# Optimization experiments

Measured on AMD Instinct MI355X. Metric: run time of the kernel, lower is better.

Reference implementation:

```python
import jax, jax.numpy as jnp
import numpy as np

ADAPTER_RATIO = 0.2


def setup_inputs() -> dict:
    key = jax.random.key(0)
    k1, k2, k3, k4, k5 = jax.random.split(key, 5)
    B, D, R, N_DOM, N_TXT = 16384, 1024, 256, 3, 1380
    image_features = jax.random.normal(k1, (B, D), dtype=jnp.float32)
    domain_labels = jax.random.randint(k2, (B,), 0, N_DOM, dtype=jnp.int64)
    W1 = jax.random.normal(k3, (N_DOM, D, R), dtype=jnp.float32) * 0.02
    W2 = jax.random.normal(k4, (N_DOM, R, D), dtype=jnp.float32) * 0.02
    txt = jax.random.normal(k5, (N_TXT, D), dtype=jnp.float32)
    # text features are L2-normalized at module init (encode_text then norm)
    text_features = txt / jnp.linalg.norm(txt, axis=-1, keepdims=True)
    logit_scale = jnp.asarray(np.log(1.0 / 0.07), dtype=jnp.float32)  # CLIP init
    return {
        "image_features": image_features,
        "domain_labels": domain_labels,
        "W1": W1,
        "W2": W2,
        "text_features": text_features,
        "logit_scale": logit_scale,
    }


def reference(image_features, domain_labels, W1, W2, text_features, logit_scale):
    # Domain-routed adapter MLP: run all n_domains experts (n is tiny), then
    # select the routed output per sample (equivalent to the per-sample loop).
    h = jax.nn.relu(jnp.einsum("bd,ndr->bnr", image_features, W1))  # [B,n,R]
    a = jax.nn.relu(jnp.einsum("bnr,nrd->bnd", h, W2))              # [B,n,D]
    idx = domain_labels[:, None, None]                                # [B,1,1]
    adapter_features = jnp.take_along_axis(a, idx, axis=1)[:, 0, :]   # [B,D]
    fused = ADAPTER_RATIO * adapter_features + (1.0 - ADAPTER_RATIO) * image_features
    fused = fused / jnp.linalg.norm(fused, axis=-1, keepdims=True)
    # text_features already normalized; concat over domains done upstream: [N_TXT, D]
    logits = jnp.exp(logit_scale) * (fused @ text_features.T)         # [B, N_TXT]
    return logits
```

## Files before the change

### kernel.cpp

```cpp
#include <hip/hip_runtime.h>
#include <hip/hip_bf16.h>
#include <math.h>

using bf16 = __hip_bfloat16;
typedef __attribute__((ext_vector_type(8))) short bf16x8;
typedef __attribute__((ext_vector_type(4))) float f32x4;
typedef __attribute__((ext_vector_type(4))) unsigned short us4;

#define GAS __attribute__((address_space(1)))
#define LAS __attribute__((address_space(3)))

__device__ __forceinline__ void gload_lds16(const bf16* g, bf16* lds) {
  __builtin_amdgcn_global_load_lds((const GAS void*)g, (LAS void*)lds, 16, 0, 0);
}
__device__ __forceinline__ float b2f(unsigned short u) {
  union { unsigned short s; bf16 b; } x; x.s = u; return __bfloat162float(x.b);
}

__global__ __launch_bounds__(256) void hist_k(const int* __restrict__ lab,
                                              int* __restrict__ blockHist) {
  const int blk = blockIdx.x, t = threadIdx.x;
  const int lane = t & 63, w = t >> 6;
  const int d = lab[blk * 256 + t];
  __shared__ int wc[4][3];
#pragma unroll
  for (int dd = 0; dd < 3; ++dd) {
    unsigned long long m = __ballot(d == dd);
    if (lane == 0) wc[w][dd] = __popcll(m);
  }
  __syncthreads();
  if (t < 3) blockHist[blk * 3 + t] = wc[0][t] + wc[1][t] + wc[2][t] + wc[3][t];
}

__global__ __launch_bounds__(256) void scan_k(const int* __restrict__ blockHist,
                                              int* __restrict__ blockOff,
                                              int* __restrict__ meta) {
  __shared__ int h[64][3];
  __shared__ int tot[3];
  const int t = threadIdx.x;
  if (t < 192) h[t / 3][t % 3] = blockHist[t];
  __syncthreads();
  if (t < 3) {
    int s = 0;
    for (int b = 0; b < 64; ++b) { int v = h[b][t]; h[b][t] = s; s += v; }
    tot[t] = s;
    meta[t] = s;
  }
  __syncthreads();
  if (t == 0) { meta[4] = 0; meta[5] = tot[0]; meta[6] = tot[0] + tot[1]; }
  if (t < 192) {
    int b = t / 3, d = t % 3;
    int base = (d == 0) ? 0 : (d == 1 ? tot[0] : tot[0] + tot[1]);
    blockOff[t] = base + h[b][d];
  }
}

__global__ __launch_bounds__(256) void scatter2_k(const int* __restrict__ lab,
                                                  const int* __restrict__ blockOff,
                                                  int* __restrict__ perm) {
  const int blk = blockIdx.x, t = threadIdx.x;
  const int lane = t & 63, w = t >> 6;
  const int i = blk * 256 + t;
  const int d = lab[i];
  __shared__ int wc[4][3];
  unsigned long long mymask = 0;
#pragma unroll
  for (int dd = 0; dd < 3; ++dd) {
    unsigned long long m = __ballot(d == dd);
    if (lane == 0) wc[w][dd] = __popcll(m);
    if (dd == d) mymask = m;
  }
  __syncthreads();
  int woff = 0;
  for (int ww = 0; ww < w; ++ww) woff += wc[ww][d];
  const unsigned long long lt = ((unsigned long long)1 << lane) - 1;
  const int rank = blockOff[blk * 3 + d] + woff + __popcll(mymask & lt);
  perm[rank] = i;
}

__global__ __launch_bounds__(256) void cvt_all_k(const float* __restrict__ x,
                                                 const float* __restrict__ W1,
                                                 const float* __restrict__ W2,
                                                 const float* __restrict__ txt,
                                                 bf16* __restrict__ Xb,
                                                 bf16* __restrict__ W1T,
                                                 bf16* __restrict__ W2T,
                                                 bf16* __restrict__ Tb) {
  const int nx = 16384 * 1024 / 4;
  const int n1 = 3 * 256 * 1024;
  const int n2 = n1 + 3 * 1024 * 256;
  const int n3 = n2 + 1536 * 1024;
  const int total = nx + n3;
  for (int i = blockIdx.x * 256 + threadIdx.x; i < total; i += 4096 * 256) {
    if (i < nx) {
      float4 v = ((const float4*)x)[i];
      bf16 t[4] = {__float2bfloat16(v.x), __float2bfloat16(v.y),
                   __float2bfloat16(v.z), __float2bfloat16(v.w)};
      ((us4*)Xb)[i] = *(const us4*)t;
      continue;
    }
    int j = i - nx;
    if (j < n1) {
      int d = j >> 18, rem = j & 262143;
      int r = rem >> 10, k = rem & 1023;
      W1T[j] = __float2bfloat16(W1[(size_t)d * 262144 + (size_t)k * 256 + r]);
    } else if (j < n2) {
      int jj = j - n1;
      int d = jj >> 18, rem = jj & 262143;
      int n = rem >> 8, k = rem & 255;
      W2T[jj] = __float2bfloat16(W2[(size_t)d * 262144 + (size_t)k * 1024 + n]);
    } else {
      int jj = j - n2;
      Tb[jj] = (jj < 1380 * 1024) ? __float2bfloat16(txt[jj]) : __float2bfloat16(0.f);
    }
  }
}

template <bool GATHER_A, int EPI, int NBLK>
__global__ __launch_bounds__(256) void gemm_bt(
    const bf16* __restrict__ A, const bf16* __restrict__ BT, bf16* __restrict__ Cv,
    const int* __restrict__ perm, const int* __restrict__ meta, int N,
    int K, int ldc, int Nvalid,
    const bf16* __restrict__ xb, float* __restrict__ ssp) {
  const int bid = blockIdx.x;
  const int xcd = bid & 7;
  const int seq = bid >> 3;
  const int nblkidx = seq % NBLK;
  const int dm = xcd + 8 * (seq / NBLK);
  const int dom = dm >> 7;
  const int mblk = dm & 127;

  const int cnt = meta[dom];
  const int base = meta[4 + dom];
  BT += (size_t)dom * N * K;

  const int m0 = mblk * 128;
  if (m0 >= cnt) return;
  const int n0 = nblkidx * 128;

  __shared__ bf16 sA[2][128][32];
  __shared__ bf16 sB[2][128][32];

  const int tid = threadIdx.x;
  const int wid = tid >> 6;
  const int lane = tid & 63;

  const int srow = (wid << 4) + (lane >> 2);
  const int skoff = (((lane & 3) ^ ((lane >> 2) & 3)) << 3);

  int p0 = m0 + srow;       if (p0 > cnt - 1) p0 = cnt - 1;
  int p1 = m0 + srow + 64;  if (p1 > cnt - 1) p1 = cnt - 1;
  long ar0, ar1;
  if (GATHER_A) { ar0 = perm[base + p0]; ar1 = perm[base + p1]; }
  else          { ar0 = base + p0;       ar1 = base + p1; }
  const bf16* a0 = A + (size_t)ar0 * K + skoff;
  const bf16* a1 = A + (size_t)ar1 * K + skoff;
  const bf16* b0 = BT + (size_t)(n0 + srow) * K + skoff;
  const bf16* b1 = BT + (size_t)(n0 + srow + 64) * K + skoff;

  const int fr = lane & 15;
  const int fq = lane >> 4;
  const int rchunk = (fq ^ (fr & 3)) << 3;

  f32x4 acc[4][4];
#pragma unroll
  for (int m = 0; m < 4; ++m)
#pragma unroll
    for (int n = 0; n < 4; ++n) acc[m][n] = (f32x4){0.f, 0.f, 0.f, 0.f};

  const int nk = K >> 5;
  auto stage = [&](int buf, int kt) {
    gload_lds16(a0 + kt * 32, &sA[buf][wid * 16][0]);
    gload_lds16(a1 + kt * 32, &sA[buf][wid * 16 + 64][0]);
    gload_lds16(b0 + kt * 32, &sB[buf][wid * 16][0]);
    gload_lds16(b1 + kt * 32, &sB[buf][wid * 16 + 64][0]);
  };

  stage(0, 0);
  __syncthreads();
  const int wr = wid >> 1, wc = wid & 1;
  for (int kt = 0; kt < nk; ++kt) {
    const int cur = kt & 1;
    if (kt + 1 < nk) stage(cur ^ 1, kt + 1);
    bf16x8 af[4], bfr[4];
#pragma unroll
    for (int m = 0; m < 4; ++m)
      af[m] = *(const bf16x8*)&sA[cur][wr * 64 + m * 16 + fr][rchunk];
#pragma unroll
    for (int n = 0; n < 4; ++n)
      bfr[n] = *(const bf16x8*)&sB[cur][wc * 64 + n * 16 + fr][rchunk];
#pragma unroll
    for (int m = 0; m < 4; ++m)
#pragma unroll
      for (int n = 0; n < 4; ++n)
        acc[m][n] = __builtin_amdgcn_mfma_f32_16x16x32_bf16(af[m], bfr[n], acc[m][n], 0, 0, 0);
    __syncthreads();
  }

  if (EPI == 0) {
#pragma unroll
    for (int m = 0; m < 4; ++m) {
#pragma unroll
      for (int r = 0; r < 4; ++r) {
        const int p = m0 + wr * 64 + m * 16 + fq * 4 + r;
        if (p < cnt) {
          const size_t crow = (size_t)(base + p);
#pragma unroll
          for (int n = 0; n < 4; ++n) {
            const int col = n0 + wc * 64 + n * 16 + fr;
            if (col < Nvalid)
              Cv[crow * (size_t)ldc + col] = __float2bfloat16(fmaxf(acc[m][n][r], 0.f));
          }
        }
      }
    }
  } else {
    __shared__ float ssred[128][2];
#pragma unroll
    for (int m = 0; m < 4; ++m) {
#pragma unroll
      for (int r = 0; r < 4; ++r) {
        const int lr = wr * 64 + m * 16 + fq * 4 + r;
        const int p = m0 + lr;
        float rowss = 0.f;
        if (p < cnt) {
          const size_t crow = (size_t)perm[base + p];
#pragma unroll
          for (int n = 0; n < 4; ++n) {
            const int col = n0 + wc * 64 + n * 16 + fr;
            const float g = 0.2f * fmaxf(acc[m][n][r], 0.f) +
                            0.8f * b2f(*(const unsigned short*)&xb[crow * 1024 + col]);
            Cv[crow * (size_t)ldc + col] = __float2bfloat16(g);
            rowss += g * g;
          }
        }
        rowss += __shfl_xor(rowss, 1, 16);
        rowss += __shfl_xor(rowss, 2, 16);
        rowss += __shfl_xor(rowss, 4, 16);
        rowss += __shfl_xor(rowss, 8, 16);
        if (fr == 0) ssred[lr][wc] = rowss;
      }
    }
    __syncthreads();
    if (tid < 128) {
      const int p = m0 + tid;
      if (p < cnt) {
        const int crow = perm[base + p];
        ssp[(size_t)nblkidx * 16384 + crow] = ssred[tid][0] + ssred[tid][1];
      }
    }
  }
}

__global__ __launch_bounds__(256, 2) void gemm3_occ(
    const bf16* __restrict__ A, const bf16* __restrict__ BT,
    float* __restrict__ C, const float* __restrict__ scale_ptr,
    const float* __restrict__ ssp) {
  extern __shared__ bf16 smem[];
  bf16* sA0 = smem;
  bf16* sB0 = smem + 16384;

  const int tid = threadIdx.x;
  const int lane = tid & 63, wid = tid >> 6;
  const int wr = wid >> 1, wc = wid & 1;
  const int fr = lane & 15, fq = lane >> 4;

  const int bid = blockIdx.x;
  const int x = bid & 7, seq = bid >> 3;
  const int mb = x * 16 + (seq >> 3), nb = seq & 7;
  const int m0 = mb << 7, n0 = nb * 192;

  auto STAGE = [&](int t) {
    const int s = t & 1, koff = t << 6;
    bf16* da = sA0 + (s << 13);
#pragma unroll
    for (int L = 0; L < 4; ++L) {
      const int idx = (L << 8) + tid;
      const int r = idx >> 3, c = idx & 7;
      gload_lds16(A + (size_t)(m0 + r) * 1024 + koff + ((c ^ (r & 7)) << 3),
                  da + ((idx & ~63) << 3));
    }
    bf16* db = sB0 + s * 12288;
#pragma unroll
    for (int L = 0; L < 6; ++L) {
      const int idx = (L << 8) + tid;
      const int r = idx >> 3, c = idx & 7;
      gload_lds16(BT + (size_t)(n0 + r) * 1024 + koff + ((c ^ (r & 7)) << 3),
                  db + ((idx & ~63) << 3));
    }
  };
  auto LDA = [&](int s, int kk, bf16x8* dst) {
    const bf16* base = sA0 + (s << 13);
#pragma unroll
    for (int m = 0; m < 4; ++m) {
      const int row = (wr << 6) + (m << 4) + fr;
      dst[m] = *(const bf16x8*)(base + (row << 6) + ((((kk << 2) + fq) ^ (fr & 7)) << 3));
    }
  };
  auto LDB = [&](int s, int kk, bf16x8* dst) {
    const bf16* base = sB0 + s * 12288;
#pragma unroll
    for (int n = 0; n < 6; ++n) {
      const int row = wc * 96 + (n << 4) + fr;
      dst[n] = *(const bf16x8*)(base + (row << 6) + ((((kk << 2) + fq) ^ (fr & 7)) << 3));
    }
  };

  f32x4 acc[4][6];
#pragma unroll
  for (int m = 0; m < 4; ++m)
#pragma unroll
    for (int n = 0; n < 6; ++n) acc[m][n] = (f32x4){0.f, 0.f, 0.f, 0.f};

  STAGE(0);
  __syncthreads();
  const int nt = 16;
  for (int t = 0; t < nt; ++t) {
    const int s = t & 1;
    if (t + 1 < nt) STAGE(t + 1);
    bf16x8 a0[4], a1[4], b0[6], b1[6];
    LDA(s, 0, a0); LDB(s, 0, b0);
    LDA(s, 1, a1); LDB(s, 1, b1);
#pragma unroll
    for (int m = 0; m < 4; ++m)
#pragma unroll
      for (int n = 0; n < 6; ++n)
        acc[m][n] = __builtin_amdgcn_mfma_f32_16x16x32_bf16(a0[m], b0[n], acc[m][n], 0, 0, 0);
#pragma unroll
    for (int m = 0; m < 4; ++m)
#pragma unroll
      for (int n = 0; n < 6; ++n)
        acc[m][n] = __builtin_amdgcn_mfma_f32_16x16x32_bf16(a1[m], b1[n], acc[m][n], 0, 0, 0);
    __syncthreads();
  }

  float* rlds = (float*)smem;
  if (tid < 128) {
    float s = 0.f;
#pragma unroll
    for (int b = 0; b < 8; ++b) s += ssp[b * 16384 + m0 + tid];
    rlds[tid] = rsqrtf(s);
  }
  __syncthreads();

  const float sc = expf(*scale_ptr);
#pragma unroll
  for (int m = 0; m < 4; ++m) {
    const int lrow = (wr << 6) + (m << 4) + (fq << 2);
    const int grow = m0 + lrow;
#pragma unroll
    for (int r = 0; r < 4; ++r) {
      const float rv = sc * rlds[lrow + r];
#pragma unroll
      for (int n = 0; n < 6; ++n) {
        const int gcol = n0 + wc * 96 + (n << 4) + fr;
        if (gcol < 1380) C[(size_t)(grow + r) * 1380 + gcol] = acc[m][n][r] * rv;
      }
    }
  }
}

extern "C" void kernel_launch(void* const* d_in, const int* in_sizes, int n_in,
                              void* d_out, int out_size, void* d_ws, size_t ws_size,
                              hipStream_t stream) {
  (void)in_sizes; (void)n_in; (void)out_size; (void)ws_size;
  const float* x    = (const float*)d_in[0];
  const int*   lab  = (const int*)d_in[1];
  const float* W1   = (const float*)d_in[2];
  const float* W2   = (const float*)d_in[3];
  const float* text = (const float*)d_in[4];
  const float* lsc  = (const float*)d_in[5];
  float* out = (float*)d_out;

  const int B = 16384, D = 1024, R = 256, NTP = 1536;

  char* p = (char*)d_ws;
  auto carve = [&](size_t bytes) {
    char* r = p;
    p += (bytes + 255) & ~(size_t)255;
    return r;
  };
  int*   meta  = (int*)carve(64);
  int*   bhist = (int*)carve(64 * 3 * 4);
  int*   boff  = (int*)carve(64 * 3 * 4);
  int*   perm  = (int*)carve((size_t)B * 4);
  float* ssp   = (float*)carve((size_t)8 * B * 4);
  bf16*  Xb    = (bf16*)carve((size_t)B * D * 2);
  bf16*  W1T   = (bf16*)carve((size_t)3 * R * D * 2);
  bf16*  W2T   = (bf16*)carve((size_t)3 * D * R * 2);
  bf16*  Tb    = (bf16*)carve((size_t)NTP * D * 2);
  bf16*  H     = (bf16*)carve((size_t)B * R * 2);
  bf16*  Fb    = (bf16*)carve((size_t)B * D * 2);

  hist_k<<<B / 256, 256, 0, stream>>>(lab, bhist);
  scan_k<<<1, 256, 0, stream>>>(bhist, boff, meta);
  scatter2_k<<<B / 256, 256, 0, stream>>>(lab, boff, perm);

  cvt_all_k<<<4096, 256, 0, stream>>>(x, W1, W2, text, Xb, W1T, W2T, Tb);

  gemm_bt<true, 0, 2><<<768, 256, 0, stream>>>(
      Xb, W1T, H, perm, meta, R, D, R, R, nullptr, nullptr);
  gemm_bt<false, 1, 8><<<3072, 256, 0, stream>>>(
      H, W2T, Fb, perm, meta, D, R, D, D, Xb, ssp);
  gemm3_occ<<<1024, 256, 81920, stream>>>(Fb, Tb, out, lsc, ssp);
}
```

Before: 162.4 us.

## Store image features in domain-sorted order and scatter only final logits

```diff
diff --git a/kernel.cpp b/kernel.cpp
--- a/kernel.cpp
+++ b/kernel.cpp
@@ -57,7 +57,8 @@
 
 __global__ __launch_bounds__(256) void scatter2_k(const int* __restrict__ lab,
                                                   const int* __restrict__ blockOff,
-                                                  int* __restrict__ perm) {
+                                                  int* __restrict__ perm,
+                                                  int* __restrict__ iperm) {
   const int blk = blockIdx.x, t = threadIdx.x;
   const int lane = t & 63, w = t >> 6;
   const int i = blk * 256 + t;
@@ -76,13 +77,15 @@
   const unsigned long long lt = ((unsigned long long)1 << lane) - 1;
   const int rank = blockOff[blk * 3 + d] + woff + __popcll(mymask & lt);
   perm[rank] = i;
+  iperm[i] = rank;
 }
 
 __global__ __launch_bounds__(256) void cvt_all_k(const float* __restrict__ x,
                                                  const float* __restrict__ W1,
                                                  const float* __restrict__ W2,
                                                  const float* __restrict__ txt,
-                                                 bf16* __restrict__ Xb,
+                                                 const int* __restrict__ iperm,
+                                                 bf16* __restrict__ Xbc,
                                                  bf16* __restrict__ W1T,
                                                  bf16* __restrict__ W2T,
                                                  bf16* __restrict__ Tb) {
@@ -93,10 +96,11 @@
   const int total = nx + n3;
   for (int i = blockIdx.x * 256 + threadIdx.x; i < total; i += 4096 * 256) {
     if (i < nx) {
+      const int row = i >> 8, c4 = i & 255;
       float4 v = ((const float4*)x)[i];
       bf16 t[4] = {__float2bfloat16(v.x), __float2bfloat16(v.y),
                    __float2bfloat16(v.z), __float2bfloat16(v.w)};
-      ((us4*)Xb)[i] = *(const us4*)t;
+      ((us4*)Xbc)[(size_t)iperm[row] * 256 + c4] = *(const us4*)t;
       continue;
     }
     int j = i - nx;
@@ -116,11 +120,10 @@
   }
 }
 
-template <bool GATHER_A, int EPI, int NBLK>
+template <int EPI, int NBLK>
 __global__ __launch_bounds__(256) void gemm_bt(
     const bf16* __restrict__ A, const bf16* __restrict__ BT, bf16* __restrict__ Cv,
-    const int* __restrict__ perm, const int* __restrict__ meta, int N,
-    int K, int ldc, int Nvalid,
+    const int* __restrict__ meta, int N, int K, int ldc, int Nvalid,
     const bf16* __restrict__ xb, float* __restrict__ ssp) {
   const int bid = blockIdx.x;
   const int xcd = bid & 7;
@@ -150,11 +153,8 @@
 
   int p0 = m0 + srow;       if (p0 > cnt - 1) p0 = cnt - 1;
   int p1 = m0 + srow + 64;  if (p1 > cnt - 1) p1 = cnt - 1;
-  long ar0, ar1;
-  if (GATHER_A) { ar0 = perm[base + p0]; ar1 = perm[base + p1]; }
-  else          { ar0 = base + p0;       ar1 = base + p1; }
-  const bf16* a0 = A + (size_t)ar0 * K + skoff;
-  const bf16* a1 = A + (size_t)ar1 * K + skoff;
+  const bf16* a0 = A + (size_t)(base + p0) * K + skoff;
+  const bf16* a1 = A + (size_t)(base + p1) * K + skoff;
   const bf16* b0 = BT + (size_t)(n0 + srow) * K + skoff;
   const bf16* b1 = BT + (size_t)(n0 + srow + 64) * K + skoff;
 
@@ -224,7 +224,7 @@
         const int p = m0 + lr;
         float rowss = 0.f;
         if (p < cnt) {
-          const size_t crow = (size_t)perm[base + p];
+          const size_t crow = (size_t)(base + p);
 #pragma unroll
           for (int n = 0; n < 4; ++n) {
             const int col = n0 + wc * 64 + n * 16 + fr;
@@ -244,10 +244,8 @@
     __syncthreads();
     if (tid < 128) {
       const int p = m0 + tid;
-      if (p < cnt) {
-        const int crow = perm[base + p];
-        ssp[(size_t)nblkidx * 16384 + crow] = ssred[tid][0] + ssred[tid][1];
-      }
+      if (p < cnt)
+        ssp[(size_t)nblkidx * 16384 + base + p] = ssred[tid][0] + ssred[tid][1];
     }
   }
 }
@@ -255,7 +253,7 @@
 __global__ __launch_bounds__(256, 2) void gemm3_occ(
     const bf16* __restrict__ A, const bf16* __restrict__ BT,
     float* __restrict__ C, const float* __restrict__ scale_ptr,
-    const float* __restrict__ ssp) {
+    const float* __restrict__ ssp, const int* __restrict__ perm) {
   extern __shared__ bf16 smem[];
   bf16* sA0 = smem;
   bf16* sB0 = smem + 16384;
@@ -335,11 +333,13 @@
   }
 
   float* rlds = (float*)smem;
+  int*   plds = (int*)((char*)smem + 512);
   if (tid < 128) {
     float s = 0.f;
 #pragma unroll
     for (int b = 0; b < 8; ++b) s += ssp[b * 16384 + m0 + tid];
     rlds[tid] = rsqrtf(s);
+    plds[tid] = perm[m0 + tid];
   }
   __syncthreads();
 
@@ -347,14 +347,14 @@
 #pragma unroll
   for (int m = 0; m < 4; ++m) {
     const int lrow = (wr << 6) + (m << 4) + (fq << 2);
-    const int grow = m0 + lrow;
 #pragma unroll
     for (int r = 0; r < 4; ++r) {
       const float rv = sc * rlds[lrow + r];
+      const size_t orow = (size_t)plds[lrow + r];
 #pragma unroll
       for (int n = 0; n < 6; ++n) {
         const int gcol = n0 + wc * 96 + (n << 4) + fr;
-        if (gcol < 1380) C[(size_t)(grow + r) * 1380 + gcol] = acc[m][n][r] * rv;
+        if (gcol < 1380) C[orow * 1380 + gcol] = acc[m][n][r] * rv;
       }
     }
   }
@@ -384,23 +384,24 @@
   int*   bhist = (int*)carve(64 * 3 * 4);
   int*   boff  = (int*)carve(64 * 3 * 4);
   int*   perm  = (int*)carve((size_t)B * 4);
+  int*   iperm = (int*)carve((size_t)B * 4);
   float* ssp   = (float*)carve((size_t)8 * B * 4);
-  bf16*  Xb    = (bf16*)carve((size_t)B * D * 2);
+  bf16*  Xbc   = (bf16*)carve((size_t)B * D * 2);
   bf16*  W1T   = (bf16*)carve((size_t)3 * R * D * 2);
   bf16*  W2T   = (bf16*)carve((size_t)3 * D * R * 2);
   bf16*  Tb    = (bf16*)carve((size_t)NTP * D * 2);
   bf16*  H     = (bf16*)carve((size_t)B * R * 2);
-  bf16*  Fb    = (bf16*)carve((size_t)B * D * 2);
+  bf16*  Fbc   = (bf16*)carve((size_t)B * D * 2);
 
   hist_k<<<B / 256, 256, 0, stream>>>(lab, bhist);
   scan_k<<<1, 256, 0, stream>>>(bhist, boff, meta);
-  scatter2_k<<<B / 256, 256, 0, stream>>>(lab, boff, perm);
-
-  cvt_all_k<<<4096, 256, 0, stream>>>(x, W1, W2, text, Xb, W1T, W2T, Tb);
-
-  gemm_bt<true, 0, 2><<<768, 256, 0, stream>>>(
-      Xb, W1T, H, perm, meta, R, D, R, R, nullptr, nullptr);
-  gemm_bt<false, 1, 8><<<3072, 256, 0, stream>>>(
-      H, W2T, Fb, perm, meta, D, R, D, D, Xb, ssp);
-  gemm3_occ<<<1024, 256, 81920, stream>>>(Fb, Tb, out, lsc, ssp);
-}
+  scatter2_k<<<B / 256, 256, 0, stream>>>(lab, boff, perm, iperm);
+
+  cvt_all_k<<<4096, 256, 0, stream>>>(x, W1, W2, text, iperm, Xbc, W1T, W2T, Tb);
+
+  gemm_bt<0, 2><<<768, 256, 0, stream>>>(
+      Xbc, W1T, H, meta, R, D, R, R, nullptr, nullptr);
+  gemm_bt<1, 8><<<3072, 256, 0, stream>>>(
+      H, W2T, Fbc, meta, D, R, D, D, Xbc, ssp);
+  gemm3_occ<<<1024, 256, 81920, stream>>>(Fbc, Tb, out, lsc, ssp, perm);
+}
```

Result: no change. 160.4 us (-1.2%).
